# Optimization experiments

Hardware: AMD Instinct MI355X
Metric: run time of the kernel (lower is better)

Reference implementation:

```python
import jax, jax.numpy as jnp
import numpy as np

N_LAYER = 4
N_HEAD = 8
D_HEAD = 64
D_MODEL = 512
D_INNER = 2048
NMT = 16  # num_mem_tokens
BSZ = 1
QLEN = 2048


def _rel_shift(x):
    # x: [i, j, b, n] -> Transformer-XL relative shift
    i, j, b, n = x.shape
    zero_pad = jnp.zeros((i, 1, b, n), dtype=x.dtype)
    x_padded = jnp.concatenate([zero_pad, x], axis=1)  # [i, j+1, b, n]
    x_padded = x_padded.reshape(j + 1, i, b, n)
    return x_padded[1:].reshape(i, j, b, n)


def _layer_norm(x, g, b):
    mu = jnp.mean(x, axis=-1, keepdims=True)
    var = jnp.mean(jnp.square(x - mu), axis=-1, keepdims=True)
    return (x - mu) / jnp.sqrt(var + 1e-5) * g + b


def setup_inputs() -> dict:
    key = jax.random.key(0)
    ks = jax.random.split(key, 12)
    s = 0.02
    return {
        "word_emb": jax.random.normal(ks[0], (BSZ, QLEN, D_MODEL), jnp.float32),
        "mem_tokens": jax.random.normal(ks[1], (NMT, BSZ, D_MODEL), jnp.float32),
        "Wqkv": jax.random.normal(ks[2], (N_LAYER, D_MODEL, 3 * N_HEAD * D_HEAD), jnp.float32) * s,
        "Wr": jax.random.normal(ks[3], (N_LAYER, D_MODEL, N_HEAD * D_HEAD), jnp.float32) * s,
        "Wo": jax.random.normal(ks[4], (N_LAYER, N_HEAD * D_HEAD, D_MODEL), jnp.float32) * s,
        "ln1_scale": jnp.ones((N_LAYER, D_MODEL), jnp.float32),
        "ln1_bias": jnp.zeros((N_LAYER, D_MODEL), jnp.float32),
        "ffn_W1": jax.random.normal(ks[5], (N_LAYER, D_MODEL, D_INNER), jnp.float32) * s,
        "ffn_b1": jnp.zeros((N_LAYER, D_INNER), jnp.float32),
        "ffn_W2": jax.random.normal(ks[6], (N_LAYER, D_INNER, D_MODEL), jnp.float32) * s,
        "ffn_b2": jnp.zeros((N_LAYER, D_MODEL), jnp.float32),
        "ln2_scale": jnp.ones((N_LAYER, D_MODEL), jnp.float32),
        "ln2_bias": jnp.zeros((N_LAYER, D_MODEL), jnp.float32),
        "r_w_bias": jax.random.normal(ks[7], (N_HEAD, D_HEAD), jnp.float32) * s,
        "r_r_bias": jax.random.normal(ks[8], (N_HEAD, D_HEAD), jnp.float32) * s,
    }


def reference(word_emb, mem_tokens, Wqkv, Wr, Wo, ln1_scale, ln1_bias,
              ffn_W1, ffn_b1, ffn_W2, ffn_b2, ln2_scale, ln2_bias,
              r_w_bias, r_r_bias):
    # word_emb: [B, Q, D] -> [Q, B, D]; prepend + append mem tokens (mem_at_end)
    w = jnp.transpose(word_emb, (1, 0, 2))
    w = jnp.concatenate([mem_tokens, w, mem_tokens], axis=0)  # [T, B, D]
    T, B = w.shape[0], w.shape[1]

    # causal mask (mlen=0) with mem-token exceptions, True = masked
    mask = jnp.triu(jnp.ones((T, T), dtype=bool), k=1)
    mask = mask.at[:NMT, :NMT].set(False)          # read-mem block attends to itself
    mask = mask.at[-NMT:, -NMT:].set(False)        # write-mem block attends to itself

    # sinusoidal relative positional embedding, pos_seq = T-1 .. 0
    inv_freq = 1.0 / (10000.0 ** (jnp.arange(0, D_MODEL, 2, dtype=jnp.float32) / D_MODEL))
    pos_seq = jnp.arange(T - 1, -1, -1.0, dtype=jnp.float32)
    sinusoid = pos_seq[:, None] * inv_freq[None, :]
    pos_emb = jnp.concatenate([jnp.sin(sinusoid), jnp.cos(sinusoid)], axis=-1)  # [T, D]

    scale = 1.0 / np.sqrt(D_HEAD)
    for l in range(N_LAYER):
        heads = w @ Wqkv[l]                                        # [T, B, 3*H*Dh]
        q, k, v = jnp.split(heads, 3, axis=-1)
        q = q.reshape(T, B, N_HEAD, D_HEAD)
        k = k.reshape(T, B, N_HEAD, D_HEAD)
        v = v.reshape(T, B, N_HEAD, D_HEAD)
        r = (pos_emb @ Wr[l]).reshape(T, N_HEAD, D_HEAD)           # [T, H, Dh]

        AC = jnp.einsum('ibnd,jbnd->ijbn', q + r_w_bias, k)
        BD = _rel_shift(jnp.einsum('ibnd,jnd->ijbn', q + r_r_bias, r))
        score = (AC + BD) * scale                                  # [T, T, B, H]
        score = jnp.where(mask[:, :, None, None], -1e30, score)
        prob = jax.nn.softmax(score, axis=1)
        attn_vec = jnp.einsum('ijbn,jbnd->ibnd', prob, v).reshape(T, B, N_HEAD * D_HEAD)

        w = _layer_norm(w + attn_vec @ Wo[l], ln1_scale[l], ln1_bias[l])  # post-LN
        ff = jax.nn.relu(w @ ffn_W1[l] + ffn_b1[l]) @ ffn_W2[l] + ffn_b2[l]
        w = _layer_norm(w + ff, ln2_scale[l], ln2_bias[l])
    return w  # [T, B, D]
```

## Files before the change

kernel.cpp:

```cpp
#include <hip/hip_runtime.h>
#include <hip/hip_bf16.h>
#include <math.h>
#include <stdint.h>

#define TT 2080
#define DM 512
#define DI 2048
#define NH 8
#define DH 64
#define NMTOK 16
#define NLAYER 4
#define QKV_N 1536
#define ATT_SCALE 0.125f
#define SPLIT 8
#define WT_STRIDE 3407872
#define QRP_HEAD 2200640

typedef short bf16x8 __attribute__((ext_vector_type(8)));
typedef float f32x4 __attribute__((ext_vector_type(4)));
typedef unsigned short ushort_t;

__device__ __forceinline__ ushort_t f2bf(float f) {
  __hip_bfloat16 h = __float2bfloat16(f);
  return *reinterpret_cast<ushort_t*>(&h);
}
__device__ __forceinline__ float bfbits2f(unsigned int hi_bits) {
  return __uint_as_float(hi_bits);
}
__device__ __forceinline__ float bf2f(ushort_t u) {
  return bfbits2f(((unsigned int)u) << 16);
}
__device__ __forceinline__ void unpack8(uint4 v, float* f) {
  f[0] = bfbits2f(v.x << 16); f[1] = bfbits2f(v.x & 0xffff0000u);
  f[2] = bfbits2f(v.y << 16); f[3] = bfbits2f(v.y & 0xffff0000u);
  f[4] = bfbits2f(v.z << 16); f[5] = bfbits2f(v.z & 0xffff0000u);
  f[6] = bfbits2f(v.w << 16); f[7] = bfbits2f(v.w & 0xffff0000u);
}
__device__ __forceinline__ unsigned int pack2(ushort_t lo, ushort_t hi) {
  return (unsigned int)lo | ((unsigned int)hi << 16);
}
__device__ __forceinline__ void barrier_lds() {
  asm volatile("s_waitcnt lgkmcnt(0)" ::: "memory");
  __builtin_amdgcn_s_barrier();
}
__device__ __forceinline__ void gload16(const ushort_t* g, ushort_t* l) {
  __builtin_amdgcn_global_load_lds(
      (__attribute__((address_space(1))) void*)(uintptr_t)g,
      (__attribute__((address_space(3))) void*)(uintptr_t)l, 16, 0, 0);
}
__device__ __forceinline__ size_t qr_rowbase(int i) {
  int m = i & 3;
  int r = (m == 0) ? 0 : (m == 1) ? 3 : (m == 2) ? 5 : 6;
  return (size_t)i * (i + 33) / 2 + 6 * (i >> 2) + r;
}
__device__ __forceinline__ size_t ft512(int r, int c) {
  return (((size_t)(r >> 4) * 16 + (c >> 5)) << 9) + (((c >> 3) & 3) << 7) +
         ((r & 15) << 3) + (c & 7);
}

__global__ __launch_bounds__(256) void k_prep(
    const float* __restrict__ Wqkv, const float* __restrict__ Wr,
    const float* __restrict__ Wo, const float* __restrict__ W1,
    const float* __restrict__ W2, ushort_t* __restrict__ dstAll,
    const float* __restrict__ we, const float* __restrict__ mem,
    float* __restrict__ w, ushort_t* __restrict__ wbft,
    ushort_t* __restrict__ posft) {
  const int tid = threadIdx.x;
  if (blockIdx.x >= 13312) {
    int idx = (blockIdx.x - 13312) * 256 + tid;
    if (idx >= TT * DM) return;
    int t = idx >> 9, d = idx & 511;
    float v;
    if (t < NMTOK) v = mem[t * DM + d];
    else if (t < NMTOK + 2048) v = we[(t - NMTOK) * DM + d];
    else v = mem[(t - (NMTOK + 2048)) * DM + d];
    w[idx] = v;
    wbft[ft512(t, d)] = f2bf(v);
    float p = (float)(TT - 1 - t);
    int i2 = d & 255;
    float freq = 1.0f / powf(10000.f, ((float)(2 * i2)) / 512.f);
    float ang = p * freq;
    posft[ft512(t, d)] = f2bf((d < 256) ? sinf(ang) : cosf(ang));
    return;
  }
  __shared__ float tl[32][33];
  const int l = blockIdx.x / 3328;
  int idx = blockIdx.x % 3328;
  const float* src;
  ushort_t* dst = dstAll + (size_t)l * WT_STRIDE;
  int K, N, local;
  bool isFT = true;
  if (idx < 768)       { src = Wqkv + (size_t)l * 512 * 1536; K = 512;  N = 1536; local = idx; }
  else if (idx < 1024) { src = Wr   + (size_t)l * 512 * 512;  dst += 786432;  K = 512;  N = 512;  local = idx - 768; }
  else if (idx < 1280) { src = Wo   + (size_t)l * 512 * 512;  dst += 1048576; K = 512;  N = 512;  local = idx - 1024; isFT = false; }
  else if (idx < 2304) { src = W1   + (size_t)l * 512 * 2048; dst += 1310720; K = 512;  N = 2048; local = idx - 1280; }
  else                 { src = W2   + (size_t)l * 2048 * 512; dst += 2359296; K = 2048; N = 512;  local = idx - 2304; }
  const int ntiles = N / 32;
  const int n0 = (local % ntiles) * 32, k0 = (local / ntiles) * 32;
#pragma unroll
  for (int p = 0; p < 4; ++p) {
    int row = (tid >> 5) + 8 * p, col = tid & 31;
    tl[row][col] = src[(size_t)(k0 + row) * N + n0 + col];
  }
  __syncthreads();
  if (isFT) {
    if (tid < 128) {
      int b = tid >> 6, l2 = tid & 63;
      int nn = b * 16 + (l2 & 15);
      int kq = (l2 >> 4) * 8;
      ushort_t t8[8];
#pragma unroll
      for (int e = 0; e < 8; ++e) t8[e] = f2bf(tl[kq + e][nn]);
      size_t ad = (((size_t)((n0 >> 4) + b) * (K >> 5) + (k0 >> 5)) << 9) +
                  ((size_t)l2 << 3);
      *(uint4*)&dst[ad] = *(uint4*)t8;
    }
  } else {
#pragma unroll
    for (int p = 0; p < 4; ++p) {
      int n = (tid >> 5) + 8 * p, k = tid & 31;
      dst[(size_t)(n0 + n) * K + k0 + k] = f2bf(tl[k][n]);
    }
  }
}

__device__ __forceinline__ void gemm32x64_body(const ushort_t* __restrict__ A,
                                               const ushort_t* __restrict__ Bt,
                                               const float* __restrict__ bias,
                                               float* __restrict__ C,
                                               ushort_t* __restrict__ Cb,
                                               int N, int K, int flags,
                                               int m0, int n0) {
  __shared__ short As[32][72];
  __shared__ short Bs[64][72];
  const int tid = threadIdx.x;
  const int lane = tid & 63, wv = tid >> 6;
  const int wm = (wv >> 1) * 16, wn = (wv & 1) * 32;
  const int lm = lane & 15, quad = lane >> 4;
  const int sr = tid >> 3, sc8 = (tid & 7) * 8;

  f32x4 acc[2];
  acc[0] = (f32x4)(0.f); acc[1] = (f32x4)(0.f);

  auto loadA = [&](int k0) -> uint4 {
    return *(const uint4*)&A[(size_t)(m0 + sr) * K + k0 + sc8];
  };
  auto loadB = [&](int row, int k0) -> uint4 {
    return *(const uint4*)&Bt[(size_t)(n0 + row) * K + k0 + sc8];
  };

  uint4 aC = loadA(0), b0C = loadB(sr, 0), b1C = loadB(sr + 32, 0);

  for (int k0 = 0; k0 < K; k0 += 64) {
    const int kn = (k0 + 64 < K) ? k0 + 64 : k0;
    uint4 aN = loadA(kn), b0N = loadB(sr, kn), b1N = loadB(sr + 32, kn);
    barrier_lds();
    *(uint4*)&As[sr][sc8] = aC;
    *(uint4*)&Bs[sr][sc8] = b0C;
    *(uint4*)&Bs[sr + 32][sc8] = b1C;
    barrier_lds();
#pragma unroll
    for (int kk = 0; kk < 64; kk += 32) {
      bf16x8 a = *(const bf16x8*)&As[wm + lm][kk + quad * 8];
      bf16x8 b0 = *(const bf16x8*)&Bs[wn + lm][kk + quad * 8];
      bf16x8 b1 = *(const bf16x8*)&Bs[wn + 16 + lm][kk + quad * 8];
      acc[0] = __builtin_amdgcn_mfma_f32_16x16x32_bf16(a, b0, acc[0], 0, 0, 0);
      acc[1] = __builtin_amdgcn_mfma_f32_16x16x32_bf16(a, b1, acc[1], 0, 0, 0);
    }
    aC = aN; b0C = b0N; b1C = b1N;
  }
#pragma unroll
  for (int nt = 0; nt < 2; ++nt) {
    int col = n0 + wn + nt * 16 + lm;
    float bv = (flags & 1) ? bias[col] : 0.f;
#pragma unroll
    for (int t = 0; t < 4; ++t) {
      int row = m0 + wm + quad * 4 + t;
      float v = acc[nt][t] + bv;
      if (flags & 2) v = fmaxf(v, 0.f);
      if (flags & 4) Cb[(size_t)row * N + col] = f2bf(v);
      else C[(size_t)row * N + col] = v;
    }
  }
}

__global__ __launch_bounds__(256) void k_gemm_mfma(const ushort_t* __restrict__ A,
                                                   const ushort_t* __restrict__ Bt,
                                                   const float* __restrict__ bias,
                                                   float* __restrict__ C,
                                                   ushort_t* __restrict__ Cb,
                                                   int N, int K, int flags) {
  gemm32x64_body(A, Bt, bias, C, Cb, N, K, flags, blockIdx.y * 32, blockIdx.x * 64);
}

__device__ __forceinline__ void gemm_ft_body(
    ushort_t* smem, const ushort_t* __restrict__ A, const ushort_t* __restrict__ Bt,
    const float* __restrict__ bias, int N, int K, int kBeg, int kEnd,
    int m0, int n0, int flags,
    float* __restrict__ Cf, ushort_t* __restrict__ Crm,
    ushort_t* __restrict__ Cft, int cftKT,
    ushort_t* __restrict__ qrb, const float* __restrict__ rrb) {
  const int tid = threadIdx.x;
  const int lane = tid & 63, wv = tid >> 6;
  const int wm = (wv >> 1) * 64, wn = (wv & 1) * 64;
  const int lm = lane & 15, quad = lane >> 4;
  const int AKT = K >> 5;
  const int mt0 = m0 >> 4, nt0 = n0 >> 4;
  const int kt0 = kBeg >> 5;

  f32x4 acc[4][4];
#pragma unroll
  for (int i = 0; i < 4; ++i)
#pragma unroll
    for (int j = 0; j < 4; ++j) acc[i][j] = (f32x4)(0.f);

  auto stage = [&](ushort_t* dA, int ktg) {
    ushort_t* dB = dA + 8192;
#pragma unroll
    for (int it = 0; it < 4; ++it) {
      const int c = (it << 8) + tid;
      const int blk = c >> 6, ln = c & 63;
      gload16(A + (((size_t)(mt0 + (blk >> 1)) * AKT + ktg + (blk & 1)) << 9) + (ln << 3),
              dA + (c << 3));
      gload16(Bt + (((size_t)(nt0 + (blk >> 1)) * AKT + ktg + (blk & 1)) << 9) + (ln << 3),
              dB + (c << 3));
    }
  };
  auto compute = [&](const ushort_t* dA) {
    const ushort_t* dB = dA + 8192;
#pragma unroll
    for (int kk = 0; kk < 2; ++kk) {
      bf16x8 a[4], b[4];
#pragma unroll
      for (int i = 0; i < 4; ++i)
        a[i] = *(const bf16x8*)&dA[((((wm >> 4) + i) << 1) + kk) * 512 + (lane << 3)];
#pragma unroll
      for (int j = 0; j < 4; ++j)
        b[j] = *(const bf16x8*)&dB[((((wn >> 4) + j) << 1) + kk) * 512 + (lane << 3)];
#pragma unroll
      for (int i = 0; i < 4; ++i)
#pragma unroll
        for (int j = 0; j < 4; ++j)
          acc[i][j] = __builtin_amdgcn_mfma_f32_16x16x32_bf16(a[i], b[j], acc[i][j], 0, 0, 0);
    }
  };

  const int nIter = (kEnd - kBeg) >> 6;
  stage(smem, kt0);
  __syncthreads();
  for (int t = 0; t < nIter; t += 2) {
    if (t + 1 < nIter) stage(smem + 16384, kt0 + (t + 1) * 2);
    compute(smem);
    __syncthreads();
    if (t + 2 < nIter) stage(smem, kt0 + (t + 2) * 2);
    compute(smem + 16384);
    __syncthreads();
  }

#pragma unroll
  for (int i = 0; i < 4; ++i) {
    const int rowb = m0 + wm + i * 16 + quad * 4;
#pragma unroll
    for (int j = 0; j < 4; ++j) {
      const int col = n0 + wn + j * 16 + lm;
      const float bv = (flags & 1) ? bias[col] : 0.f;
#pragma unroll
      for (int t2 = 0; t2 < 4; ++t2) {
        const int row = rowb + t2;
        float v = acc[i][j][t2] + bv;
        if (flags & 2) v = fmaxf(v, 0.f);
        if (Cft) {
          Cft[(((size_t)(row >> 4) * cftKT + (col >> 5)) << 9) +
              (((col >> 3) & 3) << 7) + ((row & 15) << 3) + (col & 7)] = f2bf(v);
        } else if (Crm) {
          Crm[(size_t)row * N + col] = f2bf(v);
        } else {
          Cf[(size_t)row * N + col] = v;
        }
        if (flags & 8) qrb[(size_t)row * DM + col] = f2bf(v + rrb[col]);
      }
    }
  }
}

__global__ __launch_bounds__(256) void k_gemm_qkvwr_ft(
    const ushort_t* __restrict__ wbft, const ushort_t* __restrict__ posft,
    const ushort_t* __restrict__ qkvT, const ushort_t* __restrict__ wrT,
    ushort_t* __restrict__ qkvb, ushort_t* __restrict__ rbg,
    ushort_t* __restrict__ qrb, const float* __restrict__ rrb) {
  __shared__ ushort_t smem[32768];
  int m0 = blockIdx.y * 128;
  if (m0 + 128 > TT) m0 = TT - 128;
  const int bx = blockIdx.x;
  if (bx < 12)
    gemm_ft_body(smem, wbft, qkvT, nullptr, QKV_N, DM, 0, DM, m0, bx * 128,
                 (bx < 4) ? 8 : 0, nullptr, qkvb, nullptr, 0, qrb, rrb);
  else
    gemm_ft_body(smem, posft, wrT, nullptr, DM, DM, 0, DM, m0, (bx - 12) * 128,
                 0, nullptr, rbg, nullptr, 0, nullptr, nullptr);
}

__global__ __launch_bounds__(256) void k_ffn1_ft(const ushort_t* __restrict__ wbft,
                                                 const ushort_t* __restrict__ w1T,
                                                 const float* __restrict__ b1l,
                                                 ushort_t* __restrict__ ff1ft) {
  __shared__ ushort_t smem[32768];
  int m0 = blockIdx.y * 128;
  if (m0 + 128 > TT) m0 = TT - 128;
  gemm_ft_body(smem, wbft, w1T, b1l, DI, DM, 0, DM, m0, blockIdx.x * 128,
               1 | 2, nullptr, nullptr, ff1ft, DI >> 5, nullptr, nullptr);
}

__global__ __launch_bounds__(256) void k_ffn2_ft(const ushort_t* __restrict__ ff1ft,
                                                 const ushort_t* __restrict__ w2T,
                                                 const float* __restrict__ b2l,
                                                 float* __restrict__ ff2p) {
  __shared__ ushort_t smem[32768];
  int m0 = blockIdx.y * 128;
  if (m0 + 128 > TT) m0 = TT - 128;
  const int s = blockIdx.z;
  gemm_ft_body(smem, ff1ft, w2T, b2l, DM, DI, s * 512, s * 512 + 512, m0,
               blockIdx.x * 128, (s == 0) ? 1 : 0,
               ff2p + (size_t)s * TT * DM, nullptr, nullptr, 0, nullptr, nullptr);
}

__global__ __launch_bounds__(256) void k_qr(const ushort_t* __restrict__ qrb,
                                            const ushort_t* __restrict__ rbg,
                                            ushort_t* __restrict__ qrp) {
  const int h = blockIdx.z;
  const int m0 = blockIdx.y * 32, n0 = blockIdx.x * 64;
  if (!(n0 == 0 || n0 + 63 >= TT - 32 - m0)) return;
  __shared__ short As[32][72];
  __shared__ short Bs[64][72];
  const int tid = threadIdx.x;
  const int lane = tid & 63, wv = tid >> 6;
  const int wm = (wv >> 1) * 16, wn = (wv & 1) * 32;
  const int lm = lane & 15, quad = lane >> 4;
  const int sr = tid >> 3, sc8 = (tid & 7) * 8;
  const uint4 zero4 = make_uint4(0, 0, 0, 0);

  *(uint4*)&As[sr][sc8] = *(const uint4*)&qrb[(size_t)(m0 + sr) * DM + h * DH + sc8];
  int br0 = n0 + sr, br1 = n0 + sr + 32;
  *(uint4*)&Bs[sr][sc8] =
      (br0 < TT) ? *(const uint4*)&rbg[(size_t)br0 * DM + h * DH + sc8] : zero4;
  *(uint4*)&Bs[sr + 32][sc8] =
      (br1 < TT) ? *(const uint4*)&rbg[(size_t)br1 * DM + h * DH + sc8] : zero4;
  __syncthreads();

  f32x4 acc[2];
  acc[0] = (f32x4)(0.f); acc[1] = (f32x4)(0.f);
#pragma unroll
  for (int kk = 0; kk < 64; kk += 32) {
    bf16x8 a = *(const bf16x8*)&As[wm + lm][kk + quad * 8];
    bf16x8 b0 = *(const bf16x8*)&Bs[wn + lm][kk + quad * 8];
    bf16x8 b1 = *(const bf16x8*)&Bs[wn + 16 + lm][kk + quad * 8];
    acc[0] = __builtin_amdgcn_mfma_f32_16x16x32_bf16(a, b0, acc[0], 0, 0, 0);
    acc[1] = __builtin_amdgcn_mfma_f32_16x16x32_bf16(a, b1, acc[1], 0, 0, 0);
  }
  const size_t hb = (size_t)h * QRP_HEAD;
#pragma unroll
  for (int nt = 0; nt < 2; ++nt) {
    int col = n0 + wn + nt * 16 + lm;
    if (col >= TT) continue;
#pragma unroll
    for (int t = 0; t < 4; ++t) {
      int row = m0 + wm + quad * 4 + t;
      float v = acc[nt][t];
      int p = row + col - (TT - 1);
      size_t rb = hb + qr_rowbase(row);
      if (p >= 0) qrp[rb + p] = f2bf(v);
      if (col < 16) qrp[rb + row + 1 + col] = f2bf(v);
    }
  }
}

__global__ __launch_bounds__(256) void k_attn(const ushort_t* __restrict__ qkv,
                                              const ushort_t* __restrict__ qrp,
                                              const float* __restrict__ rwb,
                                              float* __restrict__ mlP,
                                              ushort_t* __restrict__ opP) {
  const int h = blockIdx.y;
  const int qt = 64 - blockIdx.x;
  const int c = blockIdx.z;
  if (c > qt) return;
  const int i0 = qt * 32;
  const int tid = threadIdx.x;
  const int lane = tid & 63, wv = tid >> 6;
  const int lm = lane & 15, quad = lane >> 4;

  __shared__ short qw[32][72];
  __shared__ short ks_[32][72];
  __shared__ short vsT[64][70];
  __shared__ short pb[32][40];
  __shared__ float st[32][33];
  __shared__ float m_s[32], l_s[32], alpha_s[32];

  const int krr = tid >> 3, kc8 = (tid & 7) * 8;
  const int vrr = tid >> 4, vc4 = tid & 15;
  const int ii = tid >> 3, g = tid & 7, jjb = g * 4;
  const int i = i0 + ii;
  const size_t hb = (size_t)h * QRP_HEAD;
  const size_t qrRow = hb + qr_rowbase(i);
  const size_t qrRowW = hb + qr_rowbase(i + 1) + i + 2;

  auto loadK = [&](int j0) -> uint4 {
    return *(const uint4*)&qkv[(size_t)(j0 + krr) * QKV_N + DM + h * DH + kc8];
  };

  {
    uint4 qv = *(const uint4*)&qkv[(size_t)(i0 + krr) * QKV_N + h * DH + kc8];
    float f[8]; unpack8(qv, f);
    float4 w0 = *(const float4*)&rwb[h * DH + kc8];
    float4 w1 = *(const float4*)&rwb[h * DH + kc8 + 4];
    uint4 ow;
    ow.x = pack2(f2bf(f[0] + w0.x), f2bf(f[1] + w0.y));
    ow.y = pack2(f2bf(f[2] + w0.z), f2bf(f[3] + w0.w));
    ow.z = pack2(f2bf(f[4] + w1.x), f2bf(f[5] + w1.y));
    ow.w = pack2(f2bf(f[6] + w1.z), f2bf(f[7] + w1.w));
    *(uint4*)&qw[krr][kc8] = ow;
  }
  if (tid < 32) { m_s[tid] = -INFINITY; l_s[tid] = 0.f; }

  f32x4 oA = (f32x4)(0.f);
  f32x4 oB = (f32x4)(0.f);

  uint4 kcur = loadK(c * 32);
  const ushort_t* vp0 = &qkv[(size_t)(c * 32 + 2 * vrr) * QKV_N + 2 * DM + h * DH + vc4 * 4];
  uint2 v0cur = *(const uint2*)vp0, v1cur = *(const uint2*)(vp0 + QKV_N);

  for (int jt = c; jt <= qt; jt += SPLIT) {
    const int j0 = jt * 32;
    uint2 qr2 = *(const uint2*)&qrp[qrRow + j0 + jjb];
    const int jn = (jt + SPLIT <= qt) ? jt + SPLIT : jt;
    uint4 knext = loadK(jn * 32);
    const ushort_t* vpn = &qkv[(size_t)(jn * 32 + 2 * vrr) * QKV_N + 2 * DM + h * DH + vc4 * 4];
    uint2 v0n = *(const uint2*)vpn, v1n = *(const uint2*)(vpn + QKV_N);

    barrier_lds();
    *(uint4*)&ks_[krr][kc8] = kcur;
    {
      ushort_t a0 = (ushort_t)(v0cur.x & 0xffffu), a1 = (ushort_t)(v0cur.x >> 16);
      ushort_t a2 = (ushort_t)(v0cur.y & 0xffffu), a3 = (ushort_t)(v0cur.y >> 16);
      ushort_t c0 = (ushort_t)(v1cur.x & 0xffffu), c1 = (ushort_t)(v1cur.x >> 16);
      ushort_t c2 = (ushort_t)(v1cur.y & 0xffffu), c3 = (ushort_t)(v1cur.y >> 16);
      *(unsigned int*)&vsT[vc4 * 4 + 0][2 * vrr] = pack2(a0, c0);
      *(unsigned int*)&vsT[vc4 * 4 + 1][2 * vrr] = pack2(a1, c1);
      *(unsigned int*)&vsT[vc4 * 4 + 2][2 * vrr] = pack2(a2, c2);
      *(unsigned int*)&vsT[vc4 * 4 + 3][2 * vrr] = pack2(a3, c3);
    }
    barrier_lds();

    {
      const int acit = wv >> 1, acjt = wv & 1;
      f32x4 ac = (f32x4)(0.f);
#pragma unroll
      for (int k2 = 0; k2 < 64; k2 += 32) {
        bf16x8 a = *(const bf16x8*)&qw[acit * 16 + lm][k2 + quad * 8];
        bf16x8 b = *(const bf16x8*)&ks_[acjt * 16 + lm][k2 + quad * 8];
        ac = __builtin_amdgcn_mfma_f32_16x16x32_bf16(a, b, ac, 0, 0, 0);
      }
#pragma unroll
      for (int t = 0; t < 4; ++t)
        st[acit * 16 + quad * 4 + t][acjt * 16 + lm] = ac[t];
    }
    barrier_lds();

    {
      float bd4[4];
      bd4[0] = bf2f((ushort_t)(qr2.x & 0xffffu));
      bd4[1] = bf2f((ushort_t)(qr2.x >> 16));
      bd4[2] = bf2f((ushort_t)(qr2.y & 0xffffu));
      bd4[3] = bf2f((ushort_t)(qr2.y >> 16));
      float sreg[4];
#pragma unroll
      for (int u = 0; u < 4; ++u) {
        int j = j0 + jjb + u;
        float acv = st[ii][jjb + u];
        float s;
        if (j <= i) {
          s = (acv + bd4[u]) * ATT_SCALE;
        } else {
          bool inmem = (i < NMTOK && j < NMTOK) ||
                       (i >= TT - NMTOK && j >= TT - NMTOK);
          if (!inmem) s = -1e30f;
          else if (j == i + 1) s = acv * ATT_SCALE;
          else s = (acv + bf2f(qrp[qrRowW + (j - i - 2)])) * ATT_SCALE;
        }
        sreg[u] = s;
      }
      float tmax = fmaxf(fmaxf(sreg[0], sreg[1]), fmaxf(sreg[2], sreg[3]));
#pragma unroll
      for (int off = 1; off < 8; off <<= 1) tmax = fmaxf(tmax, __shfl_xor(tmax, off));
      const float mold = m_s[ii];
      const float mnew = fmaxf(mold, tmax);
      const float alpha = __expf(mold - mnew);
      float p[4], psum = 0.f;
#pragma unroll
      for (int u = 0; u < 4; ++u) { p[u] = __expf(sreg[u] - mnew); psum += p[u]; }
#pragma unroll
      for (int off = 1; off < 8; off <<= 1) psum += __shfl_xor(psum, off);
      uint2 pk;
      pk.x = pack2(f2bf(p[0]), f2bf(p[1]));
      pk.y = pack2(f2bf(p[2]), f2bf(p[3]));
      *(uint2*)&pb[ii][jjb] = pk;
      if (g == 0) {
        m_s[ii] = mnew;
        l_s[ii] = l_s[ii] * alpha + psum;
        alpha_s[ii] = alpha;
      }
    }
    barrier_lds();

    {
      float a0 = alpha_s[lm], a1 = alpha_s[16 + lm];
      union { bf16x8 v; unsigned int u[4]; } av;
      const unsigned int* vp = (const unsigned int*)&vsT[wv * 16 + lm][quad * 8];
      av.u[0] = vp[0]; av.u[1] = vp[1]; av.u[2] = vp[2]; av.u[3] = vp[3];
      bf16x8 p0 = *(const bf16x8*)&pb[lm][quad * 8];
      bf16x8 p1 = *(const bf16x8*)&pb[16 + lm][quad * 8];
#pragma unroll
      for (int t = 0; t < 4; ++t) { oA[t] *= a0; oB[t] *= a1; }
      oA = __builtin_amdgcn_mfma_f32_16x16x32_bf16(av.v, p0, oA, 0, 0, 0);
      oB = __builtin_amdgcn_mfma_f32_16x16x32_bf16(av.v, p1, oB, 0, 0, 0);
    }
    kcur = knext; v0cur = v0n; v1cur = v1n;
  }

  {
    const int pidx = (qt * NH + h) * SPLIT + c;
    if (tid < 32) {
      mlP[(size_t)pidx * 64 + tid] = m_s[tid];
      mlP[(size_t)pidx * 64 + 32 + tid] = l_s[tid];
    }
    ushort_t o0[4], o1[4];
#pragma unroll
    for (int t = 0; t < 4; ++t) { o0[t] = f2bf(oA[t]); o1[t] = f2bf(oB[t]); }
    size_t ob = (size_t)pidx * 2048;
    *(uint2*)&opP[ob + (size_t)lm * 64 + wv * 16 + quad * 4] = *(uint2*)o0;
    *(uint2*)&opP[ob + (size_t)(16 + lm) * 64 + wv * 16 + quad * 4] = *(uint2*)o1;
  }
}

__global__ __launch_bounds__(256) void k_attn_combine(const float* __restrict__ mlP,
                                                      const ushort_t* __restrict__ opP,
                                                      ushort_t* __restrict__ attnb) {
  const int qt = blockIdx.x, h = blockIdx.y;
  const int nc = (qt + 1 < SPLIT) ? qt + 1 : SPLIT;
  const int tid = threadIdx.x;
  const int i = tid >> 3, d8 = (tid & 7) * 8;
  const size_t base = (size_t)(qt * NH + h) * SPLIT;
  float m[SPLIT], l[SPLIT], wgt[SPLIT];
  float M = -INFINITY;
  for (int cc = 0; cc < nc; ++cc) {
    m[cc] = mlP[(base + cc) * 64 + i];
    l[cc] = mlP[(base + cc) * 64 + 32 + i];
    M = fmaxf(M, m[cc]);
  }
  float L = 0.f;
  for (int cc = 0; cc < nc; ++cc) { wgt[cc] = __expf(m[cc] - M); L += l[cc] * wgt[cc]; }
  float acc[8] = {0, 0, 0, 0, 0, 0, 0, 0};
  for (int cc = 0; cc < nc; ++cc) {
    uint4 v = *(const uint4*)&opP[(base + cc) * 2048 + (size_t)i * 64 + d8];
    float f[8]; unpack8(v, f);
#pragma unroll
    for (int k = 0; k < 8; ++k) acc[k] += wgt[cc] * f[k];
  }
  const float inv = 1.f / L;
  ushort_t o8[8];
#pragma unroll
  for (int k = 0; k < 8; ++k) o8[k] = f2bf(acc[k] * inv);
  *(uint4*)&attnb[(size_t)(qt * 32 + i) * DM + h * DH + d8] = *(uint4*)o8;
}

__global__ __launch_bounds__(256) void k_addln(const float* __restrict__ w,
                                               float* __restrict__ wout,
                                               ushort_t* __restrict__ wbft,
                                               const float* __restrict__ delta,
                                               int nparts,
                                               const float* __restrict__ gamma,
                                               const float* __restrict__ beta) {
  const int row = blockIdx.x;
  const int tid = threadIdx.x;
  __shared__ float red[4], red2[4];
  __shared__ float sm[512];
  size_t base = (size_t)row * DM;
  float x0 = w[base + tid];
  float x1 = w[base + tid + 256];
  for (int p = 0; p < nparts; ++p) {
    x0 += delta[(size_t)p * TT * DM + base + tid];
    x1 += delta[(size_t)p * TT * DM + base + tid + 256];
  }
  float s = x0 + x1;
#pragma unroll
  for (int off = 1; off < 64; off <<= 1) s += __shfl_xor(s, off);
  if ((tid & 63) == 0) red[tid >> 6] = s;
  __syncthreads();
  float mu = (red[0] + red[1] + red[2] + red[3]) * (1.f / 512.f);
  float d0 = x0 - mu, d1 = x1 - mu;
  float v = d0 * d0 + d1 * d1;
#pragma unroll
  for (int off = 1; off < 64; off <<= 1) v += __shfl_xor(v, off);
  if ((tid & 63) == 0) red2[tid >> 6] = v;
  __syncthreads();
  float var = (red2[0] + red2[1] + red2[2] + red2[3]) * (1.f / 512.f);
  float rstd = rsqrtf(var + 1e-5f);
  float o0 = d0 * rstd * gamma[tid] + beta[tid];
  float o1 = d1 * rstd * gamma[tid + 256] + beta[tid + 256];
  wout[base + tid] = o0;
  wout[base + tid + 256] = o1;
  sm[tid] = o0; sm[tid + 256] = o1;
  __syncthreads();
  if (tid < 64) {
    const int d8 = tid << 3;
    ushort_t t8[8];
#pragma unroll
    for (int e = 0; e < 8; ++e) t8[e] = f2bf(sm[d8 + e]);
    *(uint4*)&wbft[ft512(row, d8)] = *(uint4*)t8;
  }
}

extern "C" void kernel_launch(void* const* d_in, const int* in_sizes, int n_in,
                              void* d_out, int out_size, void* d_ws, size_t ws_size,
                              hipStream_t stream) {
  const float* we   = (const float*)d_in[0];
  const float* mem  = (const float*)d_in[1];
  const float* Wqkv = (const float*)d_in[2];
  const float* Wr   = (const float*)d_in[3];
  const float* Wo   = (const float*)d_in[4];
  const float* ln1s = (const float*)d_in[5];
  const float* ln1b = (const float*)d_in[6];
  const float* W1   = (const float*)d_in[7];
  const float* b1   = (const float*)d_in[8];
  const float* W2   = (const float*)d_in[9];
  const float* b2   = (const float*)d_in[10];
  const float* ln2s = (const float*)d_in[11];
  const float* ln2b = (const float*)d_in[12];
  const float* rwb  = (const float*)d_in[13];
  const float* rrb  = (const float*)d_in[14];

  float* w     = (float*)d_ws;
  float* proj  = w + (size_t)TT * DM;
  ushort_t* wbft  = (ushort_t*)(proj + (size_t)TT * DM);
  ushort_t* posft = wbft + (size_t)TT * DM;
  ushort_t* attnb = posft + (size_t)TT * DM;
  ushort_t* qkvb  = attnb + (size_t)TT * DM;
  ushort_t* rbg   = qkvb + (size_t)TT * QKV_N;
  ushort_t* WtAll = rbg + (size_t)TT * DM;
  ushort_t* opP   = WtAll + (size_t)NLAYER * WT_STRIDE;
  float* mlP   = (float*)(opP + (size_t)65 * 8 * SPLIT * 2048);
  ushort_t* qrb  = (ushort_t*)(mlP + (size_t)65 * 8 * SPLIT * 64);
  ushort_t* qrp  = qrb + (size_t)TT * DM;
  ushort_t* ff1ft = qkvb;
  float* ff2p  = (float*)opP;
  const size_t OFF_QKVT = 0, OFF_WRT = 786432, OFF_WOT = 1048576,
               OFF_W1T = 1310720, OFF_W2T = 2359296;

  k_prep<<<13312 + 4160, 256, 0, stream>>>(Wqkv, Wr, Wo, W1, W2, WtAll,
                                           we, mem, w, wbft, posft);

  dim3 gQW(16, 17);
  dim3 gW1(16, 17);
  dim3 gW2(4, 17, 4);
  dim3 gDM32(DM / 64, 65);
  dim3 gQR(33, 65, NH);
  dim3 gA(65, NH, SPLIT);
  dim3 gC(65, NH);

  for (int l = 0; l < NLAYER; ++l) {
    const ushort_t* Wt = WtAll + (size_t)l * WT_STRIDE;
    k_gemm_qkvwr_ft<<<gQW, 256, 0, stream>>>(wbft, posft, Wt + OFF_QKVT,
                                             Wt + OFF_WRT, qkvb, rbg, qrb, rrb);
    k_qr<<<gQR, 256, 0, stream>>>(qrb, rbg, qrp);
    k_attn<<<gA, 256, 0, stream>>>(qkvb, qrp, rwb, mlP, opP);
    k_attn_combine<<<gC, 256, 0, stream>>>(mlP, opP, attnb);
    k_gemm_mfma<<<gDM32, 256, 0, stream>>>(attnb, Wt + OFF_WOT, nullptr, proj, nullptr,
                                           DM, DM, 0);
    k_addln<<<TT, 256, 0, stream>>>(w, w, wbft, proj, 1,
                                    ln1s + (size_t)l * DM, ln1b + (size_t)l * DM);
    k_ffn1_ft<<<gW1, 256, 0, stream>>>(wbft, Wt + OFF_W1T, b1 + (size_t)l * DI, ff1ft);
    k_ffn2_ft<<<gW2, 256, 0, stream>>>(ff1ft, Wt + OFF_W2T, b2 + (size_t)l * DM, ff2p);
    float* wout = (l == NLAYER - 1) ? (float*)d_out : w;
    k_addln<<<TT, 256, 0, stream>>>(w, wout, wbft, ff2p, 4,
                                    ln2s + (size_t)l * DM, ln2b + (size_t)l * DM);
  }
}
```

Measured before the change: 662.9 us.

## Emit Q/K/V in MFMA fragment layouts and stage attention tiles via direct LDS loads

The QKV GEMM epilogue now writes Q (with r_w_bias already added), K and a transposed V straight into MFMA fragment-tiled layouts in separate buffers. The attention kernel can then stage K/V tiles with global_load_lds into double-buffered LDS. This removes the per-iteration register staging, the bias add, the V transpose and a barrier from the attention inner loop. In exchange the GEMM epilogue does scattered stores, and the loop waits on vmcnt at a full barrier each iteration.

```diff
diff --git a/kernel.cpp b/kernel.cpp
--- a/kernel.cpp
+++ b/kernel.cpp
@@ -41,6 +41,10 @@
 }
 __device__ __forceinline__ void barrier_lds() {
   asm volatile("s_waitcnt lgkmcnt(0)" ::: "memory");
+  __builtin_amdgcn_s_barrier();
+}
+__device__ __forceinline__ void barrier_all() {
+  asm volatile("s_waitcnt vmcnt(0) lgkmcnt(0)" ::: "memory");
   __builtin_amdgcn_s_barrier();
 }
 __device__ __forceinline__ void gload16(const ushort_t* g, ushort_t* l) {
@@ -196,10 +200,10 @@
 __device__ __forceinline__ void gemm_ft_body(
     ushort_t* smem, const ushort_t* __restrict__ A, const ushort_t* __restrict__ Bt,
     const float* __restrict__ bias, int N, int K, int kBeg, int kEnd,
-    int m0, int n0, int flags,
-    float* __restrict__ Cf, ushort_t* __restrict__ Crm,
-    ushort_t* __restrict__ Cft, int cftKT,
-    ushort_t* __restrict__ qrb, const float* __restrict__ rrb) {
+    int m0, int n0, int flags, int omode,
+    float* __restrict__ Cf, ushort_t* __restrict__ Cb, int cftKT,
+    ushort_t* __restrict__ aux, const float* __restrict__ rwb,
+    const float* __restrict__ rrb) {
   const int tid = threadIdx.x;
   const int lane = tid & 63, wv = tid >> 6;
   const int wm = (wv >> 1) * 64, wn = (wv & 1) * 64;
@@ -269,15 +273,23 @@
         const int row = rowb + t2;
         float v = acc[i][j][t2] + bv;
         if (flags & 2) v = fmaxf(v, 0.f);
-        if (Cft) {
-          Cft[(((size_t)(row >> 4) * cftKT + (col >> 5)) << 9) +
-              (((col >> 3) & 3) << 7) + ((row & 15) << 3) + (col & 7)] = f2bf(v);
-        } else if (Crm) {
-          Crm[(size_t)row * N + col] = f2bf(v);
+        if (omode == 0) {
+          Cf[(size_t)row * N + col] = v;
+        } else if (omode == 1) {
+          Cb[(size_t)row * N + col] = f2bf(v);
+        } else if (omode == 2) {
+          Cb[(((size_t)(row >> 4) * cftKT + (col >> 5)) << 9) +
+             (((col >> 3) & 3) << 7) + ((row & 15) << 3) + (col & 7)] = f2bf(v);
+        } else if (omode == 3) {
+          Cb[ft512(row, col)] = f2bf(v + rwb[col]);
+          aux[(size_t)row * DM + col] = f2bf(v + rrb[col]);
+        } else if (omode == 4) {
+          Cb[ft512(row, col - 512)] = f2bf(v);
         } else {
-          Cf[(size_t)row * N + col] = v;
+          const int dv = col - 1024;
+          Cb[((size_t)(dv >> 4) * 65 + (row >> 5)) * 512 +
+             (((row >> 3) & 3) << 7) + ((dv & 15) << 3) + (row & 7)] = f2bf(v);
         }
-        if (flags & 8) qrb[(size_t)row * DM + col] = f2bf(v + rrb[col]);
       }
     }
   }
@@ -286,18 +298,23 @@
 __global__ __launch_bounds__(256) void k_gemm_qkvwr_ft(
     const ushort_t* __restrict__ wbft, const ushort_t* __restrict__ posft,
     const ushort_t* __restrict__ qkvT, const ushort_t* __restrict__ wrT,
-    ushort_t* __restrict__ qkvb, ushort_t* __restrict__ rbg,
-    ushort_t* __restrict__ qrb, const float* __restrict__ rrb) {
+    ushort_t* __restrict__ qwft, ushort_t* __restrict__ kft,
+    ushort_t* __restrict__ vtft, ushort_t* __restrict__ rbg,
+    ushort_t* __restrict__ qrb, const float* __restrict__ rwb,
+    const float* __restrict__ rrb) {
   __shared__ ushort_t smem[32768];
   int m0 = blockIdx.y * 128;
   if (m0 + 128 > TT) m0 = TT - 128;
   const int bx = blockIdx.x;
-  if (bx < 12)
+  if (bx < 12) {
+    const int om = (bx < 4) ? 3 : (bx < 8 ? 4 : 5);
+    ushort_t* dst = (om == 3) ? qwft : (om == 4) ? kft : vtft;
     gemm_ft_body(smem, wbft, qkvT, nullptr, QKV_N, DM, 0, DM, m0, bx * 128,
-                 (bx < 4) ? 8 : 0, nullptr, qkvb, nullptr, 0, qrb, rrb);
-  else
+                 0, om, nullptr, dst, 0, qrb, rwb, rrb);
+  } else {
     gemm_ft_body(smem, posft, wrT, nullptr, DM, DM, 0, DM, m0, (bx - 12) * 128,
-                 0, nullptr, rbg, nullptr, 0, nullptr, nullptr);
+                 0, 1, nullptr, rbg, 0, nullptr, nullptr, nullptr);
+  }
 }
 
 __global__ __launch_bounds__(256) void k_ffn1_ft(const ushort_t* __restrict__ wbft,
@@ -308,7 +325,7 @@
   int m0 = blockIdx.y * 128;
   if (m0 + 128 > TT) m0 = TT - 128;
   gemm_ft_body(smem, wbft, w1T, b1l, DI, DM, 0, DM, m0, blockIdx.x * 128,
-               1 | 2, nullptr, nullptr, ff1ft, DI >> 5, nullptr, nullptr);
+               1 | 2, 2, nullptr, ff1ft, DI >> 5, nullptr, nullptr, nullptr);
 }
 
 __global__ __launch_bounds__(256) void k_ffn2_ft(const ushort_t* __restrict__ ff1ft,
@@ -320,8 +337,8 @@
   if (m0 + 128 > TT) m0 = TT - 128;
   const int s = blockIdx.z;
   gemm_ft_body(smem, ff1ft, w2T, b2l, DM, DI, s * 512, s * 512 + 512, m0,
-               blockIdx.x * 128, (s == 0) ? 1 : 0,
-               ff2p + (size_t)s * TT * DM, nullptr, nullptr, 0, nullptr, nullptr);
+               blockIdx.x * 128, (s == 0) ? 1 : 0, 0,
+               ff2p + (size_t)s * TT * DM, nullptr, 0, nullptr, nullptr, nullptr);
 }
 
 __global__ __launch_bounds__(256) void k_qr(const ushort_t* __restrict__ qrb,
@@ -374,9 +391,10 @@
   }
 }
 
-__global__ __launch_bounds__(256) void k_attn(const ushort_t* __restrict__ qkv,
+__global__ __launch_bounds__(256) void k_attn(const ushort_t* __restrict__ qwft,
+                                              const ushort_t* __restrict__ kft,
+                                              const ushort_t* __restrict__ vtft,
                                               const ushort_t* __restrict__ qrp,
-                                              const float* __restrict__ rwb,
                                               float* __restrict__ mlP,
                                               ushort_t* __restrict__ opP) {
   const int h = blockIdx.y;
@@ -388,75 +406,51 @@
   const int lane = tid & 63, wv = tid >> 6;
   const int lm = lane & 15, quad = lane >> 4;
 
-  __shared__ short qw[32][72];
-  __shared__ short ks_[32][72];
-  __shared__ short vsT[64][70];
-  __shared__ short pb[32][40];
-  __shared__ float st[32][33];
+  __shared__ ushort_t qwl[2048];
+  __shared__ ushort_t kl[2][2048];
+  __shared__ ushort_t vtl[2][2048];
+  __shared__ ushort_t pbl[1024];
+  __shared__ float st[32][34];
   __shared__ float m_s[32], l_s[32], alpha_s[32];
 
-  const int krr = tid >> 3, kc8 = (tid & 7) * 8;
-  const int vrr = tid >> 4, vc4 = tid & 15;
   const int ii = tid >> 3, g = tid & 7, jjb = g * 4;
   const int i = i0 + ii;
   const size_t hb = (size_t)h * QRP_HEAD;
   const size_t qrRow = hb + qr_rowbase(i);
   const size_t qrRowW = hb + qr_rowbase(i + 1) + i + 2;
 
-  auto loadK = [&](int j0) -> uint4 {
-    return *(const uint4*)&qkv[(size_t)(j0 + krr) * QKV_N + DM + h * DH + kc8];
+  const int sblk = tid >> 6, sln = tid & 63;
+  auto stageKV = [&](int j0, int buf) {
+    gload16(kft + (((size_t)((j0 >> 4) + (sblk >> 1)) * 16) + h * 2 + (sblk & 1)) * 512 +
+                (sln << 3),
+            kl[buf] + (tid << 3));
+    gload16(vtft + (((size_t)(h * 4 + sblk)) * 65 + (j0 >> 5)) * 512 + (sln << 3),
+            vtl[buf] + (tid << 3));
   };
 
-  {
-    uint4 qv = *(const uint4*)&qkv[(size_t)(i0 + krr) * QKV_N + h * DH + kc8];
-    float f[8]; unpack8(qv, f);
-    float4 w0 = *(const float4*)&rwb[h * DH + kc8];
-    float4 w1 = *(const float4*)&rwb[h * DH + kc8 + 4];
-    uint4 ow;
-    ow.x = pack2(f2bf(f[0] + w0.x), f2bf(f[1] + w0.y));
-    ow.y = pack2(f2bf(f[2] + w0.z), f2bf(f[3] + w0.w));
-    ow.z = pack2(f2bf(f[4] + w1.x), f2bf(f[5] + w1.y));
-    ow.w = pack2(f2bf(f[6] + w1.z), f2bf(f[7] + w1.w));
-    *(uint4*)&qw[krr][kc8] = ow;
-  }
+  gload16(qwft + (((size_t)((i0 >> 4) + (sblk >> 1)) * 16) + h * 2 + (sblk & 1)) * 512 +
+              (sln << 3),
+          qwl + (tid << 3));
+  stageKV(c * 32, 0);
   if (tid < 32) { m_s[tid] = -INFINITY; l_s[tid] = 0.f; }
+  barrier_all();
 
   f32x4 oA = (f32x4)(0.f);
   f32x4 oB = (f32x4)(0.f);
 
-  uint4 kcur = loadK(c * 32);
-  const ushort_t* vp0 = &qkv[(size_t)(c * 32 + 2 * vrr) * QKV_N + 2 * DM + h * DH + vc4 * 4];
-  uint2 v0cur = *(const uint2*)vp0, v1cur = *(const uint2*)(vp0 + QKV_N);
-
+  int cur = 0;
   for (int jt = c; jt <= qt; jt += SPLIT) {
     const int j0 = jt * 32;
     uint2 qr2 = *(const uint2*)&qrp[qrRow + j0 + jjb];
-    const int jn = (jt + SPLIT <= qt) ? jt + SPLIT : jt;
-    uint4 knext = loadK(jn * 32);
-    const ushort_t* vpn = &qkv[(size_t)(jn * 32 + 2 * vrr) * QKV_N + 2 * DM + h * DH + vc4 * 4];
-    uint2 v0n = *(const uint2*)vpn, v1n = *(const uint2*)(vpn + QKV_N);
-
-    barrier_lds();
-    *(uint4*)&ks_[krr][kc8] = kcur;
-    {
-      ushort_t a0 = (ushort_t)(v0cur.x & 0xffffu), a1 = (ushort_t)(v0cur.x >> 16);
-      ushort_t a2 = (ushort_t)(v0cur.y & 0xffffu), a3 = (ushort_t)(v0cur.y >> 16);
-      ushort_t c0 = (ushort_t)(v1cur.x & 0xffffu), c1 = (ushort_t)(v1cur.x >> 16);
-      ushort_t c2 = (ushort_t)(v1cur.y & 0xffffu), c3 = (ushort_t)(v1cur.y >> 16);
-      *(unsigned int*)&vsT[vc4 * 4 + 0][2 * vrr] = pack2(a0, c0);
-      *(unsigned int*)&vsT[vc4 * 4 + 1][2 * vrr] = pack2(a1, c1);
-      *(unsigned int*)&vsT[vc4 * 4 + 2][2 * vrr] = pack2(a2, c2);
-      *(unsigned int*)&vsT[vc4 * 4 + 3][2 * vrr] = pack2(a3, c3);
-    }
-    barrier_lds();
+    if (jt + SPLIT <= qt) stageKV((jt + SPLIT) * 32, cur ^ 1);
 
     {
       const int acit = wv >> 1, acjt = wv & 1;
       f32x4 ac = (f32x4)(0.f);
 #pragma unroll
-      for (int k2 = 0; k2 < 64; k2 += 32) {
-        bf16x8 a = *(const bf16x8*)&qw[acit * 16 + lm][k2 + quad * 8];
-        bf16x8 b = *(const bf16x8*)&ks_[acjt * 16 + lm][k2 + quad * 8];
+      for (int kt = 0; kt < 2; ++kt) {
+        bf16x8 a = *(const bf16x8*)&qwl[(acit * 2 + kt) * 512 + (lane << 3)];
+        bf16x8 b = *(const bf16x8*)&kl[cur][(acjt * 2 + kt) * 512 + (lane << 3)];
         ac = __builtin_amdgcn_mfma_f32_16x16x32_bf16(a, b, ac, 0, 0, 0);
       }
 #pragma unroll
@@ -502,7 +496,8 @@
       uint2 pk;
       pk.x = pack2(f2bf(p[0]), f2bf(p[1]));
       pk.y = pack2(f2bf(p[2]), f2bf(p[3]));
-      *(uint2*)&pb[ii][jjb] = pk;
+      *(uint2*)&pbl[(size_t)(ii >> 4) * 512 + (g >> 1) * 128 + (ii & 15) * 8 +
+                    (g & 1) * 4] = pk;
       if (g == 0) {
         m_s[ii] = mnew;
         l_s[ii] = l_s[ii] * alpha + psum;
@@ -513,17 +508,16 @@
 
     {
       float a0 = alpha_s[lm], a1 = alpha_s[16 + lm];
-      union { bf16x8 v; unsigned int u[4]; } av;
-      const unsigned int* vp = (const unsigned int*)&vsT[wv * 16 + lm][quad * 8];
-      av.u[0] = vp[0]; av.u[1] = vp[1]; av.u[2] = vp[2]; av.u[3] = vp[3];
-      bf16x8 p0 = *(const bf16x8*)&pb[lm][quad * 8];
-      bf16x8 p1 = *(const bf16x8*)&pb[16 + lm][quad * 8];
+      bf16x8 av = *(const bf16x8*)&vtl[cur][wv * 512 + (lane << 3)];
+      bf16x8 p0 = *(const bf16x8*)&pbl[(lane << 3)];
+      bf16x8 p1 = *(const bf16x8*)&pbl[512 + (lane << 3)];
 #pragma unroll
       for (int t = 0; t < 4; ++t) { oA[t] *= a0; oB[t] *= a1; }
-      oA = __builtin_amdgcn_mfma_f32_16x16x32_bf16(av.v, p0, oA, 0, 0, 0);
-      oB = __builtin_amdgcn_mfma_f32_16x16x32_bf16(av.v, p1, oB, 0, 0, 0);
-    }
-    kcur = knext; v0cur = v0n; v1cur = v1n;
+      oA = __builtin_amdgcn_mfma_f32_16x16x32_bf16(av, p0, oA, 0, 0, 0);
+      oB = __builtin_amdgcn_mfma_f32_16x16x32_bf16(av, p1, oB, 0, 0, 0);
+    }
+    barrier_all();
+    cur ^= 1;
   }
 
   {
@@ -643,14 +637,17 @@
   ushort_t* wbft  = (ushort_t*)(proj + (size_t)TT * DM);
   ushort_t* posft = wbft + (size_t)TT * DM;
   ushort_t* attnb = posft + (size_t)TT * DM;
-  ushort_t* qkvb  = attnb + (size_t)TT * DM;
-  ushort_t* rbg   = qkvb + (size_t)TT * QKV_N;
+  ushort_t* qkvB  = attnb + (size_t)TT * DM;
+  ushort_t* qwft  = qkvB;
+  ushort_t* kft   = qkvB + (size_t)TT * DM;
+  ushort_t* vtft  = qkvB + (size_t)2 * TT * DM;
+  ushort_t* rbg   = qkvB + (size_t)TT * QKV_N;
   ushort_t* WtAll = rbg + (size_t)TT * DM;
   ushort_t* opP   = WtAll + (size_t)NLAYER * WT_STRIDE;
   float* mlP   = (float*)(opP + (size_t)65 * 8 * SPLIT * 2048);
   ushort_t* qrb  = (ushort_t*)(mlP + (size_t)65 * 8 * SPLIT * 64);
   ushort_t* qrp  = qrb + (size_t)TT * DM;
-  ushort_t* ff1ft = qkvb;
+  ushort_t* ff1ft = qkvB;
   float* ff2p  = (float*)opP;
   const size_t OFF_QKVT = 0, OFF_WRT = 786432, OFF_WOT = 1048576,
                OFF_W1T = 1310720, OFF_W2T = 2359296;
@@ -669,9 +666,10 @@
   for (int l = 0; l < NLAYER; ++l) {
     const ushort_t* Wt = WtAll + (size_t)l * WT_STRIDE;
     k_gemm_qkvwr_ft<<<gQW, 256, 0, stream>>>(wbft, posft, Wt + OFF_QKVT,
-                                             Wt + OFF_WRT, qkvb, rbg, qrb, rrb);
+                                             Wt + OFF_WRT, qwft, kft, vtft,
+                                             rbg, qrb, rwb, rrb);
     k_qr<<<gQR, 256, 0, stream>>>(qrb, rbg, qrp);
-    k_attn<<<gA, 256, 0, stream>>>(qkvb, qrp, rwb, mlP, opP);
+    k_attn<<<gA, 256, 0, stream>>>(qwft, kft, vtft, qrp, mlP, opP);
     k_attn_combine<<<gC, 256, 0, stream>>>(mlP, opP, attnb);
     k_gemm_mfma<<<gDM32, 256, 0, stream>>>(attnb, Wt + OFF_WOT, nullptr, proj, nullptr,
                                            DM, DM, 0);
```

New measurement: 653.7 us. Within noise of the previous version (-1.4%).
